# Kernel optimization log

Measured on AMD Instinct MI355X. Metric: run time of the kernel, lower is better.

The kernel has to match this reference:

```python
import jax, jax.numpy as jnp
import numpy as np

B, S, DIN, H, K, DM, DOUT, BANK = 8, 2048, 1024, 2048, 256, 512, 1024, 4096
STICKINESS = 0.1
BANK_SCALE = 4.0
RMS_EPS = 1e-6


def setup_inputs() -> dict:
    key = jax.random.key(0)
    ks = jax.random.split(key, 8)
    s = 0.02
    prev_mode = jnp.zeros((B, K), jnp.float32).at[:, 0].set(1.0)  # default init: mode 0
    return {
        "x": jax.random.normal(ks[0], (B, S, DIN), jnp.float32),
        "prev_mode": prev_mode,
        "Wtr_w": jax.random.normal(ks[1], (DIN, H), jnp.float32) * s,
        "Wtr_b": jnp.zeros((H,), jnp.float32),
        "Wms_w": jax.random.normal(ks[2], (H, K), jnp.float32) * s,
        "Wms_b": jnp.zeros((K,), jnp.float32),
        "M": jax.random.normal(ks[3], (K, DM), jnp.float32) * 0.02,
        "g": jnp.ones((DM,), jnp.float32),
        "Wrd_w": jax.random.normal(ks[4], (DM, DOUT), jnp.float32) * s,
        "Wrd_b": jnp.zeros((DOUT,), jnp.float32),
        "bank_keys": jax.random.normal(ks[5], (BANK, DM), jnp.float32),
        "bank_vals": jax.random.normal(ks[6], (BANK, DM), jnp.float32),
        "bank_used": jnp.ones((BANK,), jnp.float32),
    }


def _l2norm(v):
    n = jnp.sqrt(jnp.sum(v * v, -1, keepdims=True))
    return v / jnp.maximum(n, 1e-12)


def reference(x, prev_mode, Wtr_w, Wtr_b, Wms_w, Wms_b, M, g, Wrd_w, Wrd_b,
              bank_keys, bank_vals, bank_used):
    # Pre-recurrence dense parts (no time dependence): [B,S,H], [B,S,K]
    h = jax.nn.relu(x @ Wtr_w + Wtr_b)
    logits = h @ Wms_w + Wms_b

    # Sequential mode selection with stickiness (eval path: hard argmax one-hot)
    def step(prev, lg):  # prev, lg: [B,K]
        m = jax.nn.one_hot(jnp.argmax(lg + STICKINESS * prev, axis=-1), K, dtype=lg.dtype)
        return m, m

    _, modes = jax.lax.scan(step, prev_mode, jnp.swapaxes(logits, 0, 1))
    modes = jnp.swapaxes(modes, 0, 1)  # [B,S,K]

    mem = modes @ M  # [B,S,DM]

    # Bank read: cosine attention over used slots (masked softmax == torch's slot filtering)
    qn = _l2norm(mem)
    kn = _l2norm(bank_keys)
    scores = jnp.einsum("bsd,nd->bsn", qn, kn) * BANK_SCALE
    scores = jnp.where(bank_used > 0.5, scores, -1e30)
    attn = jax.nn.softmax(scores, axis=-1)
    bank = jnp.einsum("bsn,nd->bsd", attn, bank_vals)

    r = mem + bank
    rn = r * (g / jnp.sqrt(jnp.mean(r * r, -1, keepdims=True) + RMS_EPS))
    y = rn @ Wrd_w + Wrd_b  # [B,S,DOUT]
    return y, modes
```

## Files before the change

kernel.cpp:

```cpp
#include <hip/hip_runtime.h>
#include <stdint.h>

#define ROWS   16384
#define KDIM   256
#define DMDIM  512
#define DOUTD  1024
#define BANKN  4096
#define DIND   1024
#define HDIMD  2048
#define FPAD   1024
#define SCHUNK 64
#define NCHK   32
#define KZ1    4
#define KZ2    8

typedef unsigned int u32;
typedef unsigned short u16;
typedef unsigned char u8;
typedef unsigned long long u64;
typedef _Float16 f16;
typedef _Float16 v8h __attribute__((ext_vector_type(8)));
typedef u16      v8u __attribute__((ext_vector_type(8)));
typedef u16      v4u __attribute__((ext_vector_type(4)));
typedef float    v4f __attribute__((ext_vector_type(4)));

__device__ __forceinline__ u32 pack_split(float v) {
    _Float16 h = (_Float16)v;
    float r = (v - (float)h) * 2048.0f;
    _Float16 l = (_Float16)r;
    u16 hs = __builtin_bit_cast(u16, h);
    u16 ls = __builtin_bit_cast(u16, l);
    return (u32)hs | ((u32)ls << 16);
}
__device__ __forceinline__ v4f mfma16(v8h a, v8h b, v4f c) {
    return __builtin_amdgcn_mfma_f32_16x16x32_f16(a, b, c, 0, 0, 0);
}
__device__ __forceinline__ void gl_lds16(const u32* g, u32* l) {
    __builtin_amdgcn_global_load_lds(g, l, 16, 0, 0);
}

template<bool OSPLIT>
__global__ __launch_bounds__(256, 2)
void gemm_mfma(const f16* __restrict__ A, const f16* __restrict__ Bm_,
               const f16* __restrict__ Br_, const float* __restrict__ bias,
               void* __restrict__ Cv, int K, int kLen)
{
    __shared__ f16 As[128 * 64];
    __shared__ f16 Bs[2 * 128 * 64];
    const int N = gridDim.x * 128;
    const int M = gridDim.y * 128;

    long gx = gridDim.x, gy = gridDim.y, gz = gridDim.z;
    long flat = ((long)blockIdx.z * gy + blockIdx.y) * gx + blockIdx.x;
    long nb = gx * gy * gz;
    long lid = (flat & 7) * (nb >> 3) + (flat >> 3);
    int bx = (int)(lid % gx);
    long t2 = lid / gx;
    int by = (int)(t2 % gy);
    int bz = (int)(t2 / gy);

    const int m0 = by * 128, n0 = bx * 128;
    const int kStart = bz * kLen;

    const int tid = threadIdx.x;
    const int lane = tid & 63, wv = tid >> 6;
    const int lx = lane & 15, q = lane >> 4;
    const int wm = (wv >> 1) * 64, wn = (wv & 1) * 64;

    const int rowb = tid >> 3;
    const int k8   = (tid & 7) ^ (rowb & 7);
    const f16* gA  = A   + (size_t)(m0 + rowb) * K + kStart + k8 * 8;
    const f16* gBm = Bm_ + (size_t)(n0 + rowb) * K + kStart + k8 * 8;
    const f16* gBr = Br_ + (size_t)(n0 + rowb) * K + kStart + k8 * 8;
    f16* lA  = As + (wv * 64) * 8;
    f16* lBm = Bs + (wv * 64) * 8;
    f16* lBr = Bs + 8192 + (wv * 64) * 8;

    int aOff[4][2], bOff[4][2];
    #pragma unroll
    for (int i = 0; i < 4; i++) {
        int ra = wm + i * 16 + lx;
        int rb = wn + i * 16 + lx;
        #pragma unroll
        for (int s = 0; s < 2; s++) {
            aOff[i][s] = ra * 128 + ((s * 64 + q * 16) ^ ((ra & 7) << 4));
            bOff[i][s] = rb * 128 + ((s * 64 + q * 16) ^ ((rb & 7) << 4));
        }
    }

    v4f acc1[4][4], acc2[4][4];
    #pragma unroll
    for (int i = 0; i < 4; i++)
        #pragma unroll
        for (int j = 0; j < 4; j++) { v4f z = {0.f, 0.f, 0.f, 0.f}; acc1[i][j] = z; acc2[i][j] = z; }

    for (int kt = 0; kt < kLen; kt += 64) {
        #pragma unroll
        for (int r = 0; r < 4; r++) {
            gl_lds16((const u32*)(gA  + (size_t)r * 32 * K), (u32*)(lA  + r * 2048));
            gl_lds16((const u32*)(gBm + (size_t)r * 32 * K), (u32*)(lBm + r * 2048));
            gl_lds16((const u32*)(gBr + (size_t)r * 32 * K), (u32*)(lBr + r * 2048));
        }
        gA += 64; gBm += 64; gBr += 64;
        __syncthreads();

        #pragma unroll
        for (int s = 0; s < 2; s++) {
            v8h am[4], bm[4], br[4];
            #pragma unroll
            for (int i = 0; i < 4; i++) {
                am[i] = *(const v8h*)((const char*)As + aOff[i][s]);
                bm[i] = *(const v8h*)((const char*)Bs + bOff[i][s]);
                br[i] = *(const v8h*)((const char*)Bs + 16384 + bOff[i][s]);
            }
            #pragma unroll
            for (int mi = 0; mi < 4; mi++)
                #pragma unroll
                for (int ni = 0; ni < 4; ni++) {
                    acc1[mi][ni] = mfma16(am[mi], bm[ni], acc1[mi][ni]);
                    acc2[mi][ni] = mfma16(am[mi], br[ni], acc2[mi][ni]);
                }
        }
        __syncthreads();
    }

    const float RS = 1.0f / 2048.0f;
    #pragma unroll
    for (int mi = 0; mi < 4; mi++) {
        #pragma unroll
        for (int ni = 0; ni < 4; ni++) {
            int col = n0 + wn + ni * 16 + lx;
            #pragma unroll
            for (int r = 0; r < 4; r++) {
                int row = m0 + wm + mi * 16 + q * 4 + r;
                float v = acc1[mi][ni][r] + acc2[mi][ni][r] * RS;
                if (OSPLIT) {
                    v += bias[col];
                    v = fmaxf(v, 0.f);
                    ((u16*)Cv)[(size_t)row * N + col] = __builtin_bit_cast(u16, (_Float16)v);
                } else {
                    ((float*)Cv)[(size_t)bz * M * N + (size_t)row * N + col] = v;
                }
            }
        }
    }
}

__global__ __launch_bounds__(256)
void packx_k(const float* __restrict__ x, u16* __restrict__ xo, long n8)
{
    long i = (long)blockIdx.x * 256 + threadIdx.x;
    if (i >= n8) return;
    const float4* xp = (const float4*)x;
    float4 a = xp[2 * i], b = xp[2 * i + 1];
    v8u o;
    o[0] = __builtin_bit_cast(u16, (_Float16)a.x);
    o[1] = __builtin_bit_cast(u16, (_Float16)a.y);
    o[2] = __builtin_bit_cast(u16, (_Float16)a.z);
    o[3] = __builtin_bit_cast(u16, (_Float16)a.w);
    o[4] = __builtin_bit_cast(u16, (_Float16)b.x);
    o[5] = __builtin_bit_cast(u16, (_Float16)b.y);
    o[6] = __builtin_bit_cast(u16, (_Float16)b.z);
    o[7] = __builtin_bit_cast(u16, (_Float16)b.w);
    *(v8u*)(xo + i * 8) = o;
}

__global__ __launch_bounds__(256)
void tsplit_k(const float* __restrict__ W, u16* __restrict__ Wm, u16* __restrict__ Wr,
              int K, int N)
{
    __shared__ u32 L[32][33];
    int k0 = blockIdx.y * 32, n0 = blockIdx.x * 32;
    int r = threadIdx.x >> 3, c4 = (threadIdx.x & 7) * 4;
    float4 v = *(const float4*)(W + (size_t)(k0 + r) * N + n0 + c4);
    L[r][c4 + 0] = pack_split(v.x);
    L[r][c4 + 1] = pack_split(v.y);
    L[r][c4 + 2] = pack_split(v.z);
    L[r][c4 + 3] = pack_split(v.w);
    __syncthreads();
    u32 o0 = L[c4 + 0][r], o1 = L[c4 + 1][r], o2 = L[c4 + 2][r], o3 = L[c4 + 3][r];
    v4u mo, ro;
    mo[0] = (u16)o0; mo[1] = (u16)o1; mo[2] = (u16)o2; mo[3] = (u16)o3;
    ro[0] = (u16)(o0 >> 16); ro[1] = (u16)(o1 >> 16); ro[2] = (u16)(o2 >> 16); ro[3] = (u16)(o3 >> 16);
    *(v4u*)(Wm + (size_t)(n0 + r) * K + k0 + c4) = mo;
    *(v4u*)(Wr + (size_t)(n0 + r) * K + k0 + c4) = ro;
}

__global__ __launch_bounds__(256)
void reduce2_k(const float* __restrict__ part, const float* __restrict__ bias,
               float* __restrict__ outp, int total4, int zStride4)
{
    int i = blockIdx.x * 256 + threadIdx.x;
    if (i >= total4) return;
    const float4* p = (const float4*)part;
    float4 s = p[i];
    #pragma unroll
    for (int z = 1; z < 4; z++) {
        float4 t = p[(size_t)z * zStride4 + i];
        s.x += t.x; s.y += t.y; s.z += t.z; s.w += t.w;
    }
    float4 b = ((const float4*)bias)[i & 63];
    s.x += b.x; s.y += b.y; s.z += b.z; s.w += b.w;
    ((float4*)outp)[i] = s;
}

template<bool BT, bool BIAS, bool RELU>
__global__ __launch_bounds__(256)
void gemm64(const float* __restrict__ A, const float* __restrict__ Bm,
            const float* __restrict__ bias, float* __restrict__ C,
            int M, int N, int K, int kLen, const int* __restrict__ mcount)
{
    if (mcount && (int)blockIdx.y * 64 >= *mcount) return;
    __shared__ float As[16][68];
    __shared__ float Bs[16][68];
    const int tid = threadIdx.x;
    const int tx = tid & 15, ty = tid >> 4;
    const int m0 = blockIdx.y * 64;
    const int n0 = blockIdx.x * 64;
    const int z  = blockIdx.z;
    const int kStart = z * kLen;
    float* Cz = C + (size_t)z * M * N;
    float acc[4][4];
    #pragma unroll
    for (int i = 0; i < 4; i++)
        #pragma unroll
        for (int j = 0; j < 4; j++) acc[i][j] = 0.f;

    for (int kt = kStart; kt < kStart + kLen; kt += 16) {
        {
            int m = tid >> 2, kq = tid & 3;
            float4 av = *(const float4*)(A + (size_t)(m0 + m) * K + kt + kq * 4);
            As[kq*4+0][m]=av.x; As[kq*4+1][m]=av.y; As[kq*4+2][m]=av.z; As[kq*4+3][m]=av.w;
        }
        if (BT) {
            int n = tid >> 2, kq = tid & 3;
            float4 bv = *(const float4*)(Bm + (size_t)(n0 + n) * K + kt + kq * 4);
            Bs[kq*4+0][n]=bv.x; Bs[kq*4+1][n]=bv.y; Bs[kq*4+2][n]=bv.z; Bs[kq*4+3][n]=bv.w;
        } else {
            int n4 = tid & 15, kk = tid >> 4;
            float4 bv = *(const float4*)(Bm + (size_t)(kt + kk) * N + n0 + n4 * 4);
            *(float4*)&Bs[kk][n4 * 4] = bv;
        }
        __syncthreads();
        #pragma unroll
        for (int k = 0; k < 16; k++) {
            float4 a0 = *(const float4*)&As[k][ty * 4];
            float4 b0 = *(const float4*)&Bs[k][tx * 4];
            float a[4] = {a0.x, a0.y, a0.z, a0.w};
            float b[4] = {b0.x, b0.y, b0.z, b0.w};
            #pragma unroll
            for (int i = 0; i < 4; i++)
                #pragma unroll
                for (int j = 0; j < 4; j++)
                    acc[i][j] = fmaf(a[i], b[j], acc[i][j]);
        }
        __syncthreads();
    }
    float4 bi = make_float4(0.f,0.f,0.f,0.f);
    if (BIAS) bi = *(const float4*)(bias + n0 + tx * 4);
    #pragma unroll
    for (int i = 0; i < 4; i++) {
        int m = m0 + ty * 4 + i;
        float o0 = acc[i][0]+bi.x, o1 = acc[i][1]+bi.y, o2 = acc[i][2]+bi.z, o3 = acc[i][3]+bi.w;
        if (RELU) { o0=fmaxf(o0,0.f); o1=fmaxf(o1,0.f); o2=fmaxf(o2,0.f); o3=fmaxf(o3,0.f); }
        *(float4*)(Cz + (size_t)m * N + n0 + tx * 4) = make_float4(o0, o1, o2, o3);
    }
}

__global__ __launch_bounds__(64)
void invkn_k(const float* __restrict__ keys, float* __restrict__ inv_kn)
{
    int n = blockIdx.x, l = threadIdx.x;
    const float4* r = (const float4*)(keys + (size_t)n * 512);
    float4 a = r[l], b = r[l + 64];
    float s = a.x*a.x + a.y*a.y + a.z*a.z + a.w*a.w
            + b.x*b.x + b.y*b.y + b.z*b.z + b.w*b.w;
    #pragma unroll
    for (int off = 32; off; off >>= 1) s += __shfl_xor(s, off);
    if (l == 0) inv_kn[n] = 1.0f / fmaxf(sqrtf(s), 1e-12f);
}

__global__ __launch_bounds__(256)
void softmax_k(const float* __restrict__ Mw, const float* __restrict__ inv_kn,
               const float* __restrict__ used, float* __restrict__ sc)
{
    const int k = blockIdx.x, tid = threadIdx.x;
    __shared__ float red[256];
    float m0 = Mw[(size_t)k*512 + tid];
    float m1 = Mw[(size_t)k*512 + 256 + tid];
    red[tid] = m0*m0 + m1*m1;
    __syncthreads();
    for (int s = 128; s > 0; s >>= 1) { if (tid < s) red[tid] += red[tid+s]; __syncthreads(); }
    float scale = 4.0f / fmaxf(sqrtf(red[0]), 1e-12f);
    __syncthreads();
    float vals[16];
    float mx = -3.0e38f;
    #pragma unroll
    for (int j = 0; j < 16; j++) {
        int n = j*256 + tid;
        float v = sc[(size_t)k*4096 + n] * scale * inv_kn[n];
        v = (used[n] > 0.5f) ? v : -1e30f;
        vals[j] = v; mx = fmaxf(mx, v);
    }
    red[tid] = mx; __syncthreads();
    for (int s = 128; s > 0; s >>= 1) { if (tid < s) red[tid] = fmaxf(red[tid], red[tid+s]); __syncthreads(); }
    mx = red[0]; __syncthreads();
    float sum = 0.f;
    #pragma unroll
    for (int j = 0; j < 16; j++) { float e = expf(vals[j] - mx); vals[j] = e; sum += e; }
    red[tid] = sum; __syncthreads();
    for (int s = 128; s > 0; s >>= 1) { if (tid < s) red[tid] += red[tid+s]; __syncthreads(); }
    float inv = 1.0f / red[0];
    #pragma unroll
    for (int j = 0; j < 16; j++) { int n = j*256 + tid; sc[(size_t)k*4096 + n] = vals[j] * inv; }
}

__global__ __launch_bounds__(256)
void redk_k(const float* __restrict__ part, float* __restrict__ outp)
{
    int idx = blockIdx.x * 256 + threadIdx.x;
    float s = 0.f;
    #pragma unroll
    for (int z = 0; z < 8; z++) s += part[(size_t)z * 131072 + idx];
    outp[idx] = s;
}

__global__ __launch_bounds__(256)
void rn_k(const float* __restrict__ Mw, const float* __restrict__ banko,
          const float* __restrict__ g, float* __restrict__ rn)
{
    int k = blockIdx.x, tid = threadIdx.x;
    __shared__ float red[256];
    float r0 = Mw[(size_t)k*512 + tid]       + banko[(size_t)k*512 + tid];
    float r1 = Mw[(size_t)k*512 + 256 + tid] + banko[(size_t)k*512 + 256 + tid];
    red[tid] = r0*r0 + r1*r1;
    __syncthreads();
    for (int s = 128; s > 0; s >>= 1) { if (tid < s) red[tid] += red[tid+s]; __syncthreads(); }
    float denom = sqrtf(red[0] * (1.0f/512.0f) + 1e-6f);
    rn[(size_t)k*512 + tid]       = r0 * (g[tid] / denom);
    rn[(size_t)k*512 + 256 + tid] = r1 * (g[256 + tid] / denom);
}

__global__ __launch_bounds__(64)
void topmask_k(const float* __restrict__ logits, u64* __restrict__ masks,
               int* __restrict__ cArr)
{
    int row = blockIdx.x, l = threadIdx.x;
    const float* lg = logits + (size_t)row * 256;
    float v0 = lg[l], v1 = lg[64 + l], v2 = lg[128 + l], v3 = lg[192 + l];
    float bv = v0; int bp = l;
    if (v1 > bv) { bv = v1; bp = 64 + l; }
    if (v2 > bv) { bv = v2; bp = 128 + l; }
    if (v3 > bv) { bv = v3; bp = 192 + l; }
    #pragma unroll
    for (int off = 32; off; off >>= 1) {
        float ov = __shfl_xor(bv, off);
        int   op = __shfl_xor(bp, off);
        if (ov > bv || (ov == bv && op < bp)) { bv = ov; bp = op; }
    }
    float t0 = v0 + 0.1f, t1 = v1 + 0.1f, t2 = v2 + 0.1f, t3 = v3 + 0.1f;
    u64 w0 = __ballot((t0 > bv) || (t0 == bv && (l)       < bp));
    u64 w1 = __ballot((t1 > bv) || (t1 == bv && (64 + l)  < bp));
    u64 w2 = __ballot((t2 > bv) || (t2 == bv && (128 + l) < bp));
    u64 w3 = __ballot((t3 > bv) || (t3 == bv && (192 + l) < bp));
    if (l == 0) {
        masks[(size_t)row*4 + 0] = w0;
        masks[(size_t)row*4 + 1] = w1;
        masks[(size_t)row*4 + 2] = w2;
        masks[(size_t)row*4 + 3] = w3;
        cArr[row] = bp;
    }
}

__global__ __launch_bounds__(64)
void flag_k(const float* __restrict__ logits, int* __restrict__ flags)
{
    int row = blockIdx.x, l = threadIdx.x;
    const float* lg = logits + (size_t)row * 256;
    float v0 = lg[l], v1 = lg[64 + l], v2 = lg[128 + l], v3 = lg[192 + l];
    float bv = v0; int bp = l;
    if (v1 > bv) { bv = v1; bp = 64 + l; }
    if (v2 > bv) { bv = v2; bp = 128 + l; }
    if (v3 > bv) { bv = v3; bp = 192 + l; }
    #pragma unroll
    for (int off = 32; off; off >>= 1) {
        float ov = __shfl_xor(bv, off);
        int   op = __shfl_xor(bp, off);
        if (ov > bv || (ov == bv && op < bp)) { bv = ov; bp = op; }
    }
    const float D = 1e-3f;
    bool r = false;
    r |= (v0 > bv - D) && ((l)       != bp);  r |= fabsf(v0 + 0.1f - bv) < D;
    r |= (v1 > bv - D) && ((64 + l)  != bp);  r |= fabsf(v1 + 0.1f - bv) < D;
    r |= (v2 > bv - D) && ((128 + l) != bp);  r |= fabsf(v2 + 0.1f - bv) < D;
    r |= (v3 > bv - D) && ((192 + l) != bp);  r |= fabsf(v3 + 0.1f - bv) < D;
    u64 any = __ballot(r);
    if (l == 0) flags[row] = (any != 0ULL) ? 1 : 0;
}

__global__ __launch_bounds__(256)
void compact_k(const int* __restrict__ flags, int* __restrict__ ridx, int* __restrict__ cnt)
{
    int row = blockIdx.x * 256 + threadIdx.x;
    if (row >= ROWS) return;
    if (flags[row]) {
        int p = atomicAdd(cnt, 1);
        if (p < FPAD) ridx[p] = row;
    }
}

__global__ __launch_bounds__(256)
void gatherx_k(const float* __restrict__ x, const int* __restrict__ ridx,
               const int* __restrict__ cnt, float* __restrict__ xg)
{
    int b = blockIdx.x;
    int n = *cnt; if (n > FPAD) n = FPAD;
    if (b >= n) return;
    int row = ridx[b];
    ((float4*)(xg + (size_t)b * 1024))[threadIdx.x] =
        ((const float4*)(x + (size_t)row * 1024))[threadIdx.x];
}

__global__ __launch_bounds__(256)
void redh_k(const float* __restrict__ part, const float* __restrict__ bias,
            const int* __restrict__ cnt, float* __restrict__ hg)
{
    int r = blockIdx.x;
    int n = *cnt; if (n > FPAD) n = FPAD;
    if (r >= n) return;
    int t = threadIdx.x;
    #pragma unroll
    for (int c0 = 0; c0 < HDIMD; c0 += 256) {
        int c = c0 + t;
        float s = part[(size_t)r * HDIMD + c];
        #pragma unroll
        for (int z = 1; z < KZ1; z++)
            s += part[(size_t)z * FPAD * HDIMD + (size_t)r * HDIMD + c];
        hg[(size_t)r * HDIMD + c] = fmaxf(s + bias[c], 0.f);
    }
}

__global__ __launch_bounds__(256)
void redL_k(const float* __restrict__ part, const float* __restrict__ bias,
            const int* __restrict__ ridx, const int* __restrict__ cnt,
            float* __restrict__ logits)
{
    int b = blockIdx.x;
    int n = *cnt; if (n > FPAD) n = FPAD;
    if (b >= n) return;
    int t = threadIdx.x;
    float s = part[(size_t)b * KDIM + t];
    #pragma unroll
    for (int z = 1; z < KZ2; z++)
        s += part[(size_t)z * FPAD * KDIM + (size_t)b * KDIM + t];
    logits[(size_t)ridx[b] * KDIM + t] = s + bias[t];
}

__global__ __launch_bounds__(64)
void scanA_k(const u64* __restrict__ masks, const int* __restrict__ cArr,
             u32* __restrict__ chmap)
{
    int blk = blockIdx.x;
    int l = threadIdx.x;
    int base = blk * 64;
    __shared__ u64 sm[64][4];
    __shared__ int sc[64];
    ulonglong2 m01 = *(const ulonglong2*)(masks + (size_t)(base + l) * 4);
    ulonglong2 m23 = *(const ulonglong2*)(masks + (size_t)(base + l) * 4 + 2);
    sm[l][0] = m01.x; sm[l][1] = m01.y; sm[l][2] = m23.x; sm[l][3] = m23.y;
    sc[l] = cArr[base + l];
    __syncthreads();

    int st[4];
    #pragma unroll
    for (int i = 0; i < 4; i++) st[i] = l * 4 + i;

    for (int j = 0; j < 64; ++j) {
        u64 w0 = sm[j][0], w1 = sm[j][1], w2 = sm[j][2], w3 = sm[j][3];
        int c = sc[j];
        #pragma unroll
        for (int i = 0; i < 4; i++) {
            int s = st[i];
            u64 wlo = (s & 64) ? w1 : w0;
            u64 whi = (s & 64) ? w3 : w2;
            u64 w   = (s & 128) ? whi : wlo;
            int stick = (int)((w >> (s & 63)) & 1ULL);
            st[i] = stick ? s : c;
        }
    }
    u32 outv = (u32)(st[0] & 255) | ((u32)(st[1] & 255) << 8)
             | ((u32)(st[2] & 255) << 16) | ((u32)(st[3] & 255) << 24);
    chmap[(size_t)blk * 64 + l] = outv;
}

__global__ __launch_bounds__(64)
void scanB_k(const u32* __restrict__ chmap, const float* __restrict__ prev_mode,
             int* __restrict__ entry)
{
    int b = blockIdx.x, l = threadIdx.x;
    __shared__ u8 lm[NCHK * 256];
    const u32* src = chmap + (size_t)b * NCHK * 64;
    #pragma unroll
    for (int i = 0; i < NCHK; ++i) ((u32*)lm)[i * 64 + l] = src[i * 64 + l];

    float4 pm = ((const float4*)(prev_mode + (size_t)b * 256))[l];
    int my = -1;
    if (pm.x > 0.5f) my = l * 4 + 0;
    if (pm.y > 0.5f) my = l * 4 + 1;
    if (pm.z > 0.5f) my = l * 4 + 2;
    if (pm.w > 0.5f) my = l * 4 + 3;
    u64 bal = __ballot(my >= 0);
    int prev = 0;
    if (bal) {
        int s2 = __ffsll(bal) - 1;
        prev = __builtin_amdgcn_readlane(my, s2);
    }
    __syncthreads();
    if (l == 0) {
        int e = prev;
        for (int ci = 0; ci < NCHK; ++ci) {
            entry[b * NCHK + ci] = e;
            e = lm[ci * 256 + e];
        }
    }
}

__global__ __launch_bounds__(64)
void scanC_k(const u64* __restrict__ masks, const int* __restrict__ cArr,
             const int* __restrict__ entry, int* __restrict__ midx)
{
    int blk = blockIdx.x, l = threadIdx.x;
    int base = blk * 64;
    ulonglong2 c01 = *(const ulonglong2*)(masks + (size_t)(base + l) * 4);
    ulonglong2 c23 = *(const ulonglong2*)(masks + (size_t)(base + l) * 4 + 2);
    int cc = cArr[base + l];
    int prev = entry[blk];
    int myres = 0;
    for (int j = 0; j < 64; ++j) {
        u64 wlo = (prev & 64) ? c01.y : c01.x;
        u64 whi = (prev & 64) ? c23.y : c23.x;
        u64 w   = (prev & 128) ? whi : wlo;
        unsigned int lo32 = (unsigned int)__builtin_amdgcn_readlane((int)(unsigned int)w, j);
        unsigned int hi32 = (unsigned int)__builtin_amdgcn_readlane((int)(unsigned int)(w >> 32), j);
        int c = __builtin_amdgcn_readlane(cc, j);
        u64 ww = ((u64)hi32 << 32) | (u64)lo32;
        int stick = (int)((ww >> (prev & 63)) & 1ULL);
        prev = stick ? prev : c;
        myres = (l == j) ? prev : myres;
    }
    midx[base + l] = myres;
}

__global__ __launch_bounds__(64)
void modesw_k(const int* __restrict__ mode_idx, float* __restrict__ modes)
{
    int r = blockIdx.x, l = threadIdx.x;
    int k = mode_idx[r];
    int base = l * 4;
    float4 v = make_float4(base == k ? 1.f : 0.f, base+1 == k ? 1.f : 0.f,
                           base+2 == k ? 1.f : 0.f, base+3 == k ? 1.f : 0.f);
    ((float4*)(modes + (size_t)r * 256))[l] = v;
}

__global__ __launch_bounds__(256)
void ygather_k(const int* __restrict__ mode_idx, const float* __restrict__ ytab,
               float* __restrict__ y)
{
    int r = blockIdx.x;
    int k = mode_idx[r];
    const float4* src = (const float4*)(ytab + (size_t)k * 1024);
    float4* dst = (float4*)(y + (size_t)r * 1024);
    dst[threadIdx.x] = src[threadIdx.x];
}

extern "C" void kernel_launch(void* const* d_in, const int* in_sizes, int n_in,
                              void* d_out, int out_size, void* d_ws, size_t ws_size,
                              hipStream_t stream)
{
    const float* x       = (const float*)d_in[0];
    const float* prevm   = (const float*)d_in[1];
    const float* Wtr_w   = (const float*)d_in[2];
    const float* Wtr_b   = (const float*)d_in[3];
    const float* Wms_w   = (const float*)d_in[4];
    const float* Wms_b   = (const float*)d_in[5];
    const float* Mw      = (const float*)d_in[6];
    const float* g       = (const float*)d_in[7];
    const float* Wrd_w   = (const float*)d_in[8];
    const float* Wrd_b   = (const float*)d_in[9];
    const float* bkeys   = (const float*)d_in[10];
    const float* bvals   = (const float*)d_in[11];
    const float* bused   = (const float*)d_in[12];

    float* y_out     = (float*)d_out;
    float* modes_out = y_out + (size_t)ROWS * DOUTD;

    char* w = (char*)d_ws;
    size_t o = 0;
    auto alloc = [&](size_t b) { size_t r = o; o = (o + b + 255) & ~(size_t)255; return r; };

    size_t oLog  = alloc((size_t)ROWS * 256 * 4);
    size_t oMask = alloc((size_t)ROWS * 32);
    size_t oCar  = alloc((size_t)ROWS * 4);
    size_t oMidx = alloc((size_t)ROWS * 4);
    size_t oInv  = alloc((size_t)BANKN * 4);
    size_t oSc   = alloc((size_t)256 * 4096 * 4);
    size_t oPB   = alloc((size_t)8 * 256 * 512 * 4);
    size_t oBo   = alloc((size_t)256 * 512 * 4);
    size_t oRn   = alloc((size_t)256 * 512 * 4);
    size_t oYt   = alloc((size_t)256 * 1024 * 4);
    size_t oW1m  = alloc((size_t)HDIMD * DIND * 2);
    size_t oW1r  = alloc((size_t)HDIMD * DIND * 2);
    size_t oW2m  = alloc((size_t)KDIM * HDIMD * 2);
    size_t oW2r  = alloc((size_t)KDIM * HDIMD * 2);
    size_t oChm  = alloc((size_t)8 * NCHK * 256);
    size_t oEnt  = alloc((size_t)8 * NCHK * 4);
    size_t oFlag = alloc((size_t)ROWS * 4);
    size_t oRidx = alloc((size_t)FPAD * 4);
    size_t oCnt  = alloc(256);
    size_t oXg   = alloc((size_t)FPAD * DIND * 4);
    size_t oHP   = alloc((size_t)KZ1 * FPAD * HDIMD * 4);
    size_t oHg   = alloc((size_t)FPAD * HDIMD * 4);
    size_t oLP   = alloc((size_t)KZ2 * FPAD * KDIM * 4);
    size_t persist = o;

    int CM = 256;
    const int cands[7] = {16384, 8192, 4096, 2048, 1024, 512, 256};
    for (int i = 0; i < 7; i++) {
        size_t need = persist + (size_t)cands[i] * 10240 + 1024;
        if (need <= ws_size) { CM = cands[i]; break; }
    }
    size_t oXi = alloc((size_t)CM * DIND * 2);
    size_t oHi = alloc((size_t)CM * HDIMD * 2);
    size_t oP2 = alloc((size_t)4 * CM * 256 * 4);

    float* logits = (float*)(w + oLog);
    u64*   masks  = (u64*)(w + oMask);
    int*   cArr   = (int*)(w + oCar);
    int*   midx   = (int*)(w + oMidx);
    float* invkn  = (float*)(w + oInv);
    float* scores = (float*)(w + oSc);
    float* partB  = (float*)(w + oPB);
    float* banko  = (float*)(w + oBo);
    float* rn     = (float*)(w + oRn);
    float* ytab   = (float*)(w + oYt);
    u16*   W1m    = (u16*)(w + oW1m);
    u16*   W1r    = (u16*)(w + oW1r);
    u16*   W2m    = (u16*)(w + oW2m);
    u16*   W2r    = (u16*)(w + oW2r);
    u32*   chmap  = (u32*)(w + oChm);
    int*   entry  = (int*)(w + oEnt);
    int*   flags  = (int*)(w + oFlag);
    int*   ridx   = (int*)(w + oRidx);
    int*   cnt    = (int*)(w + oCnt);
    float* xg     = (float*)(w + oXg);
    float* hPart  = (float*)(w + oHP);
    float* hg     = (float*)(w + oHg);
    float* lPart  = (float*)(w + oLP);
    u16*   xi     = (u16*)(w + oXi);
    u16*   hi     = (u16*)(w + oHi);
    float* part2  = (float*)(w + oP2);

    invkn_k<<<BANKN, 64, 0, stream>>>(bkeys, invkn);
    gemm64<true, false, false><<<dim3(64, 4, 1), 256, 0, stream>>>(Mw, bkeys, nullptr, scores,
                                                                   256, 4096, 512, 512, nullptr);
    softmax_k<<<KDIM, 256, 0, stream>>>(Mw, invkn, bused, scores);
    gemm64<false, false, false><<<dim3(8, 4, 8), 256, 0, stream>>>(scores, bvals, nullptr, partB,
                                                                   256, 512, 4096, 512, nullptr);
    redk_k<<<512, 256, 0, stream>>>(partB, banko);
    rn_k<<<KDIM, 256, 0, stream>>>(Mw, banko, g, rn);
    gemm64<false, true, false><<<dim3(16, 4, 1), 256, 0, stream>>>(rn, Wrd_w, Wrd_b, ytab,
                                                                   256, 1024, 512, 512, nullptr);

    tsplit_k<<<dim3(HDIMD / 32, DIND / 32), 256, 0, stream>>>(Wtr_w, W1m, W1r, DIND, HDIMD);
    tsplit_k<<<dim3(KDIM / 32, HDIMD / 32), 256, 0, stream>>>(Wms_w, W2m, W2r, HDIMD, KDIM);

    for (int ch0 = 0; ch0 < ROWS; ch0 += CM) {
        long n8 = (long)CM * DIND / 8;
        packx_k<<<(int)((n8 + 255) / 256), 256, 0, stream>>>(x + (size_t)ch0 * DIND, xi, n8);
        gemm_mfma<true><<<dim3(HDIMD / 128, CM / 128, 1), 256, 0, stream>>>(
            (const f16*)xi, (const f16*)W1m, (const f16*)W1r, Wtr_b, hi, DIND, DIND);
        gemm_mfma<false><<<dim3(KDIM / 128, CM / 128, 4), 256, 0, stream>>>(
            (const f16*)hi, (const f16*)W2m, (const f16*)W2r, nullptr, part2, HDIMD, HDIMD / 4);
        int total4 = CM * 256 / 4;
        reduce2_k<<<(total4 + 255) / 256, 256, 0, stream>>>(part2, Wms_b,
            logits + (size_t)ch0 * 256, total4, total4);
    }

    flag_k<<<ROWS, 64, 0, stream>>>(logits, flags);
    hipMemsetAsync(cnt, 0, 4, stream);
    compact_k<<<ROWS / 256, 256, 0, stream>>>(flags, ridx, cnt);
    gatherx_k<<<FPAD, 256, 0, stream>>>(x, ridx, cnt, xg);
    gemm64<false, false, false><<<dim3(HDIMD / 64, FPAD / 64, KZ1), 256, 0, stream>>>(
        xg, Wtr_w, nullptr, hPart, FPAD, HDIMD, DIND, DIND / KZ1, cnt);
    redh_k<<<FPAD, 256, 0, stream>>>(hPart, Wtr_b, cnt, hg);
    gemm64<false, false, false><<<dim3(KDIM / 64, FPAD / 64, KZ2), 256, 0, stream>>>(
        hg, Wms_w, nullptr, lPart, FPAD, KDIM, HDIMD, HDIMD / KZ2, cnt);
    redL_k<<<FPAD, 256, 0, stream>>>(lPart, Wms_b, ridx, cnt, logits);

    topmask_k<<<ROWS, 64, 0, stream>>>(logits, masks, cArr);
    scanA_k<<<8 * NCHK, 64, 0, stream>>>(masks, cArr, chmap);
    scanB_k<<<8, 64, 0, stream>>>(chmap, prevm, entry);
    scanC_k<<<8 * NCHK, 64, 0, stream>>>(masks, cArr, entry, midx);

    modesw_k<<<ROWS, 64, 0, stream>>>(midx, modes_out);
    ygather_k<<<ROWS, 256, 0, stream>>>(midx, ytab, y_out);
}
```

Measured before the change: 592.6 us.

## Move bank-read GEMMs to split-fp16 MFMA and halve split-K for logits

```diff
diff --git a/kernel.cpp b/kernel.cpp
--- a/kernel.cpp
+++ b/kernel.cpp
@@ -11,7 +11,7 @@
 #define FPAD   1024
 #define SCHUNK 64
 #define NCHK   32
-#define KZ1    4
+#define KZ1    2
 #define KZ2    8
 
 typedef unsigned int u32;
@@ -20,6 +20,7 @@
 typedef unsigned long long u64;
 typedef _Float16 f16;
 typedef _Float16 v8h __attribute__((ext_vector_type(8)));
+typedef short    v8s __attribute__((ext_vector_type(8)));
 typedef u16      v8u __attribute__((ext_vector_type(8)));
 typedef u16      v4u __attribute__((ext_vector_type(4)));
 typedef float    v4f __attribute__((ext_vector_type(4)));
@@ -31,6 +32,18 @@
     u16 hs = __builtin_bit_cast(u16, h);
     u16 ls = __builtin_bit_cast(u16, l);
     return (u32)hs | ((u32)ls << 16);
+}
+__device__ __forceinline__ v8h unpL(uint4 a, uint4 b) {
+    v8s s1 = __builtin_bit_cast(v8s, a);
+    v8s s2 = __builtin_bit_cast(v8s, b);
+    v8s lo = __builtin_shufflevector(s1, s2, 0, 2, 4, 6, 8, 10, 12, 14);
+    return __builtin_bit_cast(v8h, lo);
+}
+__device__ __forceinline__ v8h unpH(uint4 a, uint4 b) {
+    v8s s1 = __builtin_bit_cast(v8s, a);
+    v8s s2 = __builtin_bit_cast(v8s, b);
+    v8s hi = __builtin_shufflevector(s1, s2, 1, 3, 5, 7, 9, 11, 13, 15);
+    return __builtin_bit_cast(v8h, hi);
 }
 __device__ __forceinline__ v4f mfma16(v8h a, v8h b, v4f c) {
     return __builtin_amdgcn_mfma_f32_16x16x32_f16(a, b, c, 0, 0, 0);
@@ -146,6 +159,104 @@
     }
 }
 
+template<bool BIASF>
+__global__ __launch_bounds__(256, 2)
+void gemm_sp3(const u32* __restrict__ A, const u32* __restrict__ Bt,
+              const float* __restrict__ bias, float* __restrict__ Cv,
+              int K, int kLen)
+{
+    __shared__ u32 As[4096];
+    __shared__ u32 Bs[4096];
+    const int N = gridDim.x * 128;
+    const int M = gridDim.y * 128;
+
+    long gx = gridDim.x, gy = gridDim.y, gz = gridDim.z;
+    long flat = ((long)blockIdx.z * gy + blockIdx.y) * gx + blockIdx.x;
+    long nb = gx * gy * gz;
+    long lid = (flat & 7) * (nb >> 3) + (flat >> 3);
+    int bx = (int)(lid % gx);
+    long t2 = lid / gx;
+    int by = (int)(t2 % gy);
+    int bz = (int)(t2 / gy);
+
+    const int m0 = by * 128, n0 = bx * 128;
+    const int kStart = bz * kLen;
+
+    const int tid = threadIdx.x;
+    const int lane = tid & 63, wv = tid >> 6;
+    const int lx = lane & 15, q = lane >> 4;
+    const int wm = (wv >> 1) * 64, wn = (wv & 1) * 64;
+
+    const u32* gA = A + (size_t)(m0 + (tid >> 6) * 8 + (tid & 7)) * K + kStart + ((tid >> 3) & 7) * 4;
+    const u32* gB = Bt + (size_t)(n0 + (tid >> 6) * 8 + (tid & 7)) * K + kStart + ((tid >> 3) & 7) * 4;
+    u32* lA = As + (wv * 64) * 4;
+    u32* lB = Bs + (wv * 64) * 4;
+
+    int caOff[4], cbOff[4];
+    #pragma unroll
+    for (int i = 0; i < 4; i++) {
+        int m = wm + i * 16 + lx;
+        caOff[i] = (((m >> 3) * 64) + q * 16 + (m & 7)) * 4;
+        int n = wn + i * 16 + lx;
+        cbOff[i] = (((n >> 3) * 64) + q * 16 + (n & 7)) * 4;
+    }
+
+    v4f acc1[4][4], acc2[4][4];
+    #pragma unroll
+    for (int i = 0; i < 4; i++)
+        #pragma unroll
+        for (int j = 0; j < 4; j++) { v4f z = {0.f, 0.f, 0.f, 0.f}; acc1[i][j] = z; acc2[i][j] = z; }
+
+    for (int kt = 0; kt < kLen; kt += 32) {
+        #pragma unroll
+        for (int r = 0; r < 4; r++) {
+            gl_lds16(gA + (size_t)r * 32 * K, lA + r * 1024);
+            gl_lds16(gB + (size_t)r * 32 * K, lB + r * 1024);
+        }
+        gA += 32; gB += 32;
+        __syncthreads();
+
+        v8h am[4], ar[4], bm[4], br[4];
+        #pragma unroll
+        for (int i = 0; i < 4; i++) {
+            uint4 x1 = *(const uint4*)(As + caOff[i]);
+            uint4 x2 = *(const uint4*)(As + caOff[i] + 32);
+            am[i] = unpL(x1, x2); ar[i] = unpH(x1, x2);
+            uint4 y1 = *(const uint4*)(Bs + cbOff[i]);
+            uint4 y2 = *(const uint4*)(Bs + cbOff[i] + 32);
+            bm[i] = unpL(y1, y2); br[i] = unpH(y1, y2);
+        }
+        #pragma unroll
+        for (int mi = 0; mi < 4; mi++)
+            #pragma unroll
+            for (int ni = 0; ni < 4; ni++) {
+                acc1[mi][ni] = mfma16(am[mi], bm[ni], acc1[mi][ni]);
+                acc2[mi][ni] = mfma16(am[mi], br[ni], acc2[mi][ni]);
+                acc2[mi][ni] = mfma16(ar[mi], bm[ni], acc2[mi][ni]);
+            }
+        __syncthreads();
+    }
+
+    const float RS = 1.0f / 2048.0f;
+    #pragma unroll
+    for (int mi = 0; mi < 4; mi++) {
+        #pragma unroll
+        for (int ni = 0; ni < 4; ni++) {
+            int col = n0 + wn + ni * 16 + lx;
+            #pragma unroll
+            for (int r = 0; r < 4; r++) {
+                int row = m0 + wm + mi * 16 + q * 4 + r;
+                float v = acc1[mi][ni][r] + acc2[mi][ni][r] * RS;
+                if (BIASF) {
+                    Cv[(size_t)row * N + col] = v + bias[col];
+                } else {
+                    Cv[(size_t)bz * M * N + (size_t)row * N + col] = v;
+                }
+            }
+        }
+    }
+}
+
 __global__ __launch_bounds__(256)
 void packx_k(const float* __restrict__ x, u16* __restrict__ xo, long n8)
 {
@@ -163,6 +274,35 @@
     o[6] = __builtin_bit_cast(u16, (_Float16)b.z);
     o[7] = __builtin_bit_cast(u16, (_Float16)b.w);
     *(v8u*)(xo + i * 8) = o;
+}
+
+__global__ __launch_bounds__(256)
+void packrow_k(const float* __restrict__ x, u32* __restrict__ xi, long n4)
+{
+    long i = (long)blockIdx.x * 256 + threadIdx.x;
+    if (i >= n4) return;
+    float4 v = ((const float4*)x)[i];
+    uint4 o;
+    o.x = pack_split(v.x); o.y = pack_split(v.y);
+    o.z = pack_split(v.z); o.w = pack_split(v.w);
+    ((uint4*)xi)[i] = o;
+}
+
+__global__ __launch_bounds__(256)
+void tpack_k(const float* __restrict__ W, u32* __restrict__ Wt, int K, int N)
+{
+    __shared__ u32 L[32][33];
+    int k0 = blockIdx.y * 32, n0 = blockIdx.x * 32;
+    int r = threadIdx.x >> 3, c4 = (threadIdx.x & 7) * 4;
+    float4 v = *(const float4*)(W + (size_t)(k0 + r) * N + n0 + c4);
+    L[r][c4 + 0] = pack_split(v.x);
+    L[r][c4 + 1] = pack_split(v.y);
+    L[r][c4 + 2] = pack_split(v.z);
+    L[r][c4 + 3] = pack_split(v.w);
+    __syncthreads();
+    uint4 ov;
+    ov.x = L[c4 + 0][r]; ov.y = L[c4 + 1][r]; ov.z = L[c4 + 2][r]; ov.w = L[c4 + 3][r];
+    *(uint4*)(Wt + (size_t)(n0 + r) * K + k0 + c4) = ov;
 }
 
 __global__ __launch_bounds__(256)
@@ -188,14 +328,13 @@
 
 __global__ __launch_bounds__(256)
 void reduce2_k(const float* __restrict__ part, const float* __restrict__ bias,
-               float* __restrict__ outp, int total4, int zStride4)
+               float* __restrict__ outp, int total4, int zStride4, int zc)
 {
     int i = blockIdx.x * 256 + threadIdx.x;
     if (i >= total4) return;
     const float4* p = (const float4*)part;
     float4 s = p[i];
-    #pragma unroll
-    for (int z = 1; z < 4; z++) {
+    for (int z = 1; z < zc; z++) {
         float4 t = p[(size_t)z * zStride4 + i];
         s.x += t.x; s.y += t.y; s.z += t.z; s.w += t.w;
     }
@@ -612,6 +751,12 @@
     size_t oW1r  = alloc((size_t)HDIMD * DIND * 2);
     size_t oW2m  = alloc((size_t)KDIM * HDIMD * 2);
     size_t oW2r  = alloc((size_t)KDIM * HDIMD * 2);
+    size_t oMwP  = alloc((size_t)KDIM * DMDIM * 4);
+    size_t oBkP  = alloc((size_t)BANKN * DMDIM * 4);
+    size_t oAtP  = alloc((size_t)KDIM * BANKN * 4);
+    size_t oBvP  = alloc((size_t)DMDIM * BANKN * 4);
+    size_t oRnP  = alloc((size_t)KDIM * DMDIM * 4);
+    size_t oWrdP = alloc((size_t)DOUTD * DMDIM * 4);
     size_t oChm  = alloc((size_t)8 * NCHK * 256);
     size_t oEnt  = alloc((size_t)8 * NCHK * 4);
     size_t oFlag = alloc((size_t)ROWS * 4);
@@ -626,12 +771,12 @@
     int CM = 256;
     const int cands[7] = {16384, 8192, 4096, 2048, 1024, 512, 256};
     for (int i = 0; i < 7; i++) {
-        size_t need = persist + (size_t)cands[i] * 10240 + 1024;
+        size_t need = persist + (size_t)cands[i] * 8192 + 1024;
         if (need <= ws_size) { CM = cands[i]; break; }
     }
     size_t oXi = alloc((size_t)CM * DIND * 2);
     size_t oHi = alloc((size_t)CM * HDIMD * 2);
-    size_t oP2 = alloc((size_t)4 * CM * 256 * 4);
+    size_t oP2 = alloc((size_t)2 * CM * 256 * 4);
 
     float* logits = (float*)(w + oLog);
     u64*   masks  = (u64*)(w + oMask);
@@ -647,6 +792,12 @@
     u16*   W1r    = (u16*)(w + oW1r);
     u16*   W2m    = (u16*)(w + oW2m);
     u16*   W2r    = (u16*)(w + oW2r);
+    u32*   MwP    = (u32*)(w + oMwP);
+    u32*   bkP    = (u32*)(w + oBkP);
+    u32*   atP    = (u32*)(w + oAtP);
+    u32*   bvP    = (u32*)(w + oBvP);
+    u32*   rnP    = (u32*)(w + oRnP);
+    u32*   WrdP   = (u32*)(w + oWrdP);
     u32*   chmap  = (u32*)(w + oChm);
     int*   entry  = (int*)(w + oEnt);
     int*   flags  = (int*)(w + oFlag);
@@ -661,15 +812,21 @@
     float* part2  = (float*)(w + oP2);
 
     invkn_k<<<BANKN, 64, 0, stream>>>(bkeys, invkn);
-    gemm64<true, false, false><<<dim3(64, 4, 1), 256, 0, stream>>>(Mw, bkeys, nullptr, scores,
-                                                                   256, 4096, 512, 512, nullptr);
+    packrow_k<<<(KDIM * DMDIM / 4 + 255) / 256, 256, 0, stream>>>(Mw, MwP, KDIM * DMDIM / 4);
+    packrow_k<<<(BANKN * DMDIM / 4 + 255) / 256, 256, 0, stream>>>(bkeys, bkP, BANKN * DMDIM / 4);
+    tpack_k<<<dim3(DMDIM / 32, BANKN / 32), 256, 0, stream>>>(bvals, bvP, BANKN, DMDIM);
+    tpack_k<<<dim3(DOUTD / 32, DMDIM / 32), 256, 0, stream>>>(Wrd_w, WrdP, DMDIM, DOUTD);
+    gemm_sp3<false><<<dim3(BANKN / 128, KDIM / 128, 1), 256, 0, stream>>>(
+        MwP, bkP, nullptr, scores, DMDIM, DMDIM);
     softmax_k<<<KDIM, 256, 0, stream>>>(Mw, invkn, bused, scores);
-    gemm64<false, false, false><<<dim3(8, 4, 8), 256, 0, stream>>>(scores, bvals, nullptr, partB,
-                                                                   256, 512, 4096, 512, nullptr);
+    packrow_k<<<(KDIM * BANKN / 4 + 255) / 256, 256, 0, stream>>>(scores, atP, KDIM * BANKN / 4);
+    gemm_sp3<false><<<dim3(DMDIM / 128, KDIM / 128, 8), 256, 0, stream>>>(
+        atP, bvP, nullptr, partB, BANKN, BANKN / 8);
     redk_k<<<512, 256, 0, stream>>>(partB, banko);
     rn_k<<<KDIM, 256, 0, stream>>>(Mw, banko, g, rn);
-    gemm64<false, true, false><<<dim3(16, 4, 1), 256, 0, stream>>>(rn, Wrd_w, Wrd_b, ytab,
-                                                                   256, 1024, 512, 512, nullptr);
+    packrow_k<<<(KDIM * DMDIM / 4 + 255) / 256, 256, 0, stream>>>(rn, rnP, KDIM * DMDIM / 4);
+    gemm_sp3<true><<<dim3(DOUTD / 128, KDIM / 128, 1), 256, 0, stream>>>(
+        rnP, WrdP, Wrd_b, ytab, DMDIM, DMDIM);
 
     tsplit_k<<<dim3(HDIMD / 32, DIND / 32), 256, 0, stream>>>(Wtr_w, W1m, W1r, DIND, HDIMD);
     tsplit_k<<<dim3(KDIM / 32, HDIMD / 32), 256, 0, stream>>>(Wms_w, W2m, W2r, HDIMD, KDIM);
@@ -679,11 +836,11 @@
         packx_k<<<(int)((n8 + 255) / 256), 256, 0, stream>>>(x + (size_t)ch0 * DIND, xi, n8);
         gemm_mfma<true><<<dim3(HDIMD / 128, CM / 128, 1), 256, 0, stream>>>(
             (const f16*)xi, (const f16*)W1m, (const f16*)W1r, Wtr_b, hi, DIND, DIND);
-        gemm_mfma<false><<<dim3(KDIM / 128, CM / 128, 4), 256, 0, stream>>>(
-            (const f16*)hi, (const f16*)W2m, (const f16*)W2r, nullptr, part2, HDIMD, HDIMD / 4);
+        gemm_mfma<false><<<dim3(KDIM / 128, CM / 128, 2), 256, 0, stream>>>(
+            (const f16*)hi, (const f16*)W2m, (const f16*)W2r, nullptr, part2, HDIMD, HDIMD / 2);
         int total4 = CM * 256 / 4;
         reduce2_k<<<(total4 + 255) / 256, 256, 0, stream>>>(part2, Wms_b,
-            logits + (size_t)ch0 * 256, total4, total4);
+            logits + (size_t)ch0 * 256, total4, total4, 2);
     }
 
     flag_k<<<ROWS, 64, 0, stream>>>(logits, flags);
```

New measurement: 624.2 us. 1.05x slower.

## Fuse fp32-to-fp16 conversion into GEMM A-load and merge small row kernels

Applied to the files above, without the earlier changes.

```diff
diff --git a/kernel.cpp b/kernel.cpp
--- a/kernel.cpp
+++ b/kernel.cpp
@@ -39,9 +39,9 @@
     __builtin_amdgcn_global_load_lds(g, l, 16, 0, 0);
 }
 
-template<bool OSPLIT>
+template<bool OSPLIT, bool AF32>
 __global__ __launch_bounds__(256, 2)
-void gemm_mfma(const f16* __restrict__ A, const f16* __restrict__ Bm_,
+void gemm_mfma(const void* __restrict__ Av, const f16* __restrict__ Bm_,
                const f16* __restrict__ Br_, const float* __restrict__ bias,
                void* __restrict__ Cv, int K, int kLen)
 {
@@ -69,12 +69,14 @@
 
     const int rowb = tid >> 3;
     const int k8   = (tid & 7) ^ (rowb & 7);
-    const f16* gA  = A   + (size_t)(m0 + rowb) * K + kStart + k8 * 8;
+    const f16*  gA  = AF32 ? nullptr : (const f16*)Av + (size_t)(m0 + rowb) * K + kStart + k8 * 8;
+    const float* gAf = AF32 ? (const float*)Av + (size_t)(m0 + rowb) * K + kStart + (tid & 7) * 8 : nullptr;
     const f16* gBm = Bm_ + (size_t)(n0 + rowb) * K + kStart + k8 * 8;
     const f16* gBr = Br_ + (size_t)(n0 + rowb) * K + kStart + k8 * 8;
     f16* lA  = As + (wv * 64) * 8;
     f16* lBm = Bs + (wv * 64) * 8;
     f16* lBr = Bs + 8192 + (wv * 64) * 8;
+    const int aw = rowb * 64 + k8 * 8;
 
     int aOff[4][2], bOff[4][2];
     #pragma unroll
@@ -95,13 +97,42 @@
         for (int j = 0; j < 4; j++) { v4f z = {0.f, 0.f, 0.f, 0.f}; acc1[i][j] = z; acc2[i][j] = z; }
 
     for (int kt = 0; kt < kLen; kt += 64) {
-        #pragma unroll
-        for (int r = 0; r < 4; r++) {
-            gl_lds16((const u32*)(gA  + (size_t)r * 32 * K), (u32*)(lA  + r * 2048));
-            gl_lds16((const u32*)(gBm + (size_t)r * 32 * K), (u32*)(lBm + r * 2048));
-            gl_lds16((const u32*)(gBr + (size_t)r * 32 * K), (u32*)(lBr + r * 2048));
-        }
-        gA += 64; gBm += 64; gBr += 64;
+        if (AF32) {
+            float4 fa[4][2];
+            #pragma unroll
+            for (int r = 0; r < 4; r++) {
+                fa[r][0] = *(const float4*)(gAf + (size_t)r * 32 * K);
+                fa[r][1] = *(const float4*)(gAf + (size_t)r * 32 * K + 4);
+            }
+            gAf += 64;
+            #pragma unroll
+            for (int r = 0; r < 4; r++) {
+                gl_lds16((const u32*)(gBm + (size_t)r * 32 * K), (u32*)(lBm + r * 2048));
+                gl_lds16((const u32*)(gBr + (size_t)r * 32 * K), (u32*)(lBr + r * 2048));
+            }
+            #pragma unroll
+            for (int r = 0; r < 4; r++) {
+                v8u o;
+                o[0] = __builtin_bit_cast(u16, (_Float16)fa[r][0].x);
+                o[1] = __builtin_bit_cast(u16, (_Float16)fa[r][0].y);
+                o[2] = __builtin_bit_cast(u16, (_Float16)fa[r][0].z);
+                o[3] = __builtin_bit_cast(u16, (_Float16)fa[r][0].w);
+                o[4] = __builtin_bit_cast(u16, (_Float16)fa[r][1].x);
+                o[5] = __builtin_bit_cast(u16, (_Float16)fa[r][1].y);
+                o[6] = __builtin_bit_cast(u16, (_Float16)fa[r][1].z);
+                o[7] = __builtin_bit_cast(u16, (_Float16)fa[r][1].w);
+                *(v8u*)(As + aw + r * 2048) = o;
+            }
+        } else {
+            #pragma unroll
+            for (int r = 0; r < 4; r++) {
+                gl_lds16((const u32*)(gA  + (size_t)r * 32 * K), (u32*)(lA  + r * 2048));
+                gl_lds16((const u32*)(gBm + (size_t)r * 32 * K), (u32*)(lBm + r * 2048));
+                gl_lds16((const u32*)(gBr + (size_t)r * 32 * K), (u32*)(lBr + r * 2048));
+            }
+            gA += 64;
+        }
+        gBm += 64; gBr += 64;
         __syncthreads();
 
         #pragma unroll
@@ -144,25 +175,6 @@
             }
         }
     }
-}
-
-__global__ __launch_bounds__(256)
-void packx_k(const float* __restrict__ x, u16* __restrict__ xo, long n8)
-{
-    long i = (long)blockIdx.x * 256 + threadIdx.x;
-    if (i >= n8) return;
-    const float4* xp = (const float4*)x;
-    float4 a = xp[2 * i], b = xp[2 * i + 1];
-    v8u o;
-    o[0] = __builtin_bit_cast(u16, (_Float16)a.x);
-    o[1] = __builtin_bit_cast(u16, (_Float16)a.y);
-    o[2] = __builtin_bit_cast(u16, (_Float16)a.z);
-    o[3] = __builtin_bit_cast(u16, (_Float16)a.w);
-    o[4] = __builtin_bit_cast(u16, (_Float16)b.x);
-    o[5] = __builtin_bit_cast(u16, (_Float16)b.y);
-    o[6] = __builtin_bit_cast(u16, (_Float16)b.z);
-    o[7] = __builtin_bit_cast(u16, (_Float16)b.w);
-    *(v8u*)(xo + i * 8) = o;
 }
 
 __global__ __launch_bounds__(256)
@@ -188,14 +200,13 @@
 
 __global__ __launch_bounds__(256)
 void reduce2_k(const float* __restrict__ part, const float* __restrict__ bias,
-               float* __restrict__ outp, int total4, int zStride4)
+               float* __restrict__ outp, int total4, int zStride4, int zc)
 {
     int i = blockIdx.x * 256 + threadIdx.x;
     if (i >= total4) return;
     const float4* p = (const float4*)part;
     float4 s = p[i];
-    #pragma unroll
-    for (int z = 1; z < 4; z++) {
+    for (int z = 1; z < zc; z++) {
         float4 t = p[(size_t)z * zStride4 + i];
         s.x += t.x; s.y += t.y; s.z += t.z; s.w += t.w;
     }
@@ -342,8 +353,8 @@
 }
 
 __global__ __launch_bounds__(64)
-void topmask_k(const float* __restrict__ logits, u64* __restrict__ masks,
-               int* __restrict__ cArr)
+void topflag_k(const float* __restrict__ logits, u64* __restrict__ masks,
+               int* __restrict__ cArr, int* __restrict__ flags)
 {
     int row = blockIdx.x, l = threadIdx.x;
     const float* lg = logits + (size_t)row * 256;
@@ -363,39 +374,21 @@
     u64 w1 = __ballot((t1 > bv) || (t1 == bv && (64 + l)  < bp));
     u64 w2 = __ballot((t2 > bv) || (t2 == bv && (128 + l) < bp));
     u64 w3 = __ballot((t3 > bv) || (t3 == bv && (192 + l) < bp));
+    const float D = 1e-3f;
+    bool r = false;
+    r |= (v0 > bv - D) && ((l)       != bp);  r |= fabsf(t0 - bv) < D;
+    r |= (v1 > bv - D) && ((64 + l)  != bp);  r |= fabsf(t1 - bv) < D;
+    r |= (v2 > bv - D) && ((128 + l) != bp);  r |= fabsf(t2 - bv) < D;
+    r |= (v3 > bv - D) && ((192 + l) != bp);  r |= fabsf(t3 - bv) < D;
+    u64 any = __ballot(r);
     if (l == 0) {
         masks[(size_t)row*4 + 0] = w0;
         masks[(size_t)row*4 + 1] = w1;
         masks[(size_t)row*4 + 2] = w2;
         masks[(size_t)row*4 + 3] = w3;
         cArr[row] = bp;
-    }
-}
-
-__global__ __launch_bounds__(64)
-void flag_k(const float* __restrict__ logits, int* __restrict__ flags)
-{
-    int row = blockIdx.x, l = threadIdx.x;
-    const float* lg = logits + (size_t)row * 256;
-    float v0 = lg[l], v1 = lg[64 + l], v2 = lg[128 + l], v3 = lg[192 + l];
-    float bv = v0; int bp = l;
-    if (v1 > bv) { bv = v1; bp = 64 + l; }
-    if (v2 > bv) { bv = v2; bp = 128 + l; }
-    if (v3 > bv) { bv = v3; bp = 192 + l; }
-    #pragma unroll
-    for (int off = 32; off; off >>= 1) {
-        float ov = __shfl_xor(bv, off);
-        int   op = __shfl_xor(bp, off);
-        if (ov > bv || (ov == bv && op < bp)) { bv = ov; bp = op; }
-    }
-    const float D = 1e-3f;
-    bool r = false;
-    r |= (v0 > bv - D) && ((l)       != bp);  r |= fabsf(v0 + 0.1f - bv) < D;
-    r |= (v1 > bv - D) && ((64 + l)  != bp);  r |= fabsf(v1 + 0.1f - bv) < D;
-    r |= (v2 > bv - D) && ((128 + l) != bp);  r |= fabsf(v2 + 0.1f - bv) < D;
-    r |= (v3 > bv - D) && ((192 + l) != bp);  r |= fabsf(v3 + 0.1f - bv) < D;
-    u64 any = __ballot(r);
-    if (l == 0) flags[row] = (any != 0ULL) ? 1 : 0;
+        flags[row] = (any != 0ULL) ? 1 : 0;
+    }
 }
 
 __global__ __launch_bounds__(256)
@@ -551,26 +544,20 @@
     midx[base + l] = myres;
 }
 
-__global__ __launch_bounds__(64)
-void modesw_k(const int* __restrict__ mode_idx, float* __restrict__ modes)
-{
-    int r = blockIdx.x, l = threadIdx.x;
+__global__ __launch_bounds__(256)
+void yout_k(const int* __restrict__ mode_idx, const float* __restrict__ ytab,
+            float* __restrict__ y, float* __restrict__ modes)
+{
+    int r = blockIdx.x, t = threadIdx.x;
     int k = mode_idx[r];
-    int base = l * 4;
-    float4 v = make_float4(base == k ? 1.f : 0.f, base+1 == k ? 1.f : 0.f,
-                           base+2 == k ? 1.f : 0.f, base+3 == k ? 1.f : 0.f);
-    ((float4*)(modes + (size_t)r * 256))[l] = v;
-}
-
-__global__ __launch_bounds__(256)
-void ygather_k(const int* __restrict__ mode_idx, const float* __restrict__ ytab,
-               float* __restrict__ y)
-{
-    int r = blockIdx.x;
-    int k = mode_idx[r];
-    const float4* src = (const float4*)(ytab + (size_t)k * 1024);
-    float4* dst = (float4*)(y + (size_t)r * 1024);
-    dst[threadIdx.x] = src[threadIdx.x];
+    ((float4*)(y + (size_t)r * 1024))[t] =
+        ((const float4*)(ytab + (size_t)k * 1024))[t];
+    if (t < 64) {
+        int base = t * 4;
+        float4 v = make_float4(base == k ? 1.f : 0.f, base+1 == k ? 1.f : 0.f,
+                               base+2 == k ? 1.f : 0.f, base+3 == k ? 1.f : 0.f);
+        ((float4*)(modes + (size_t)r * 256))[t] = v;
+    }
 }
 
 extern "C" void kernel_launch(void* const* d_in, const int* in_sizes, int n_in,
@@ -626,10 +613,9 @@
     int CM = 256;
     const int cands[7] = {16384, 8192, 4096, 2048, 1024, 512, 256};
     for (int i = 0; i < 7; i++) {
-        size_t need = persist + (size_t)cands[i] * 10240 + 1024;
+        size_t need = persist + (size_t)cands[i] * 8192 + 1024;
         if (need <= ws_size) { CM = cands[i]; break; }
     }
-    size_t oXi = alloc((size_t)CM * DIND * 2);
     size_t oHi = alloc((size_t)CM * HDIMD * 2);
     size_t oP2 = alloc((size_t)4 * CM * 256 * 4);
 
@@ -656,7 +642,6 @@
     float* hPart  = (float*)(w + oHP);
     float* hg     = (float*)(w + oHg);
     float* lPart  = (float*)(w + oLP);
-    u16*   xi     = (u16*)(w + oXi);
     u16*   hi     = (u16*)(w + oHi);
     float* part2  = (float*)(w + oP2);
 
@@ -675,18 +660,17 @@
     tsplit_k<<<dim3(KDIM / 32, HDIMD / 32), 256, 0, stream>>>(Wms_w, W2m, W2r, HDIMD, KDIM);
 
     for (int ch0 = 0; ch0 < ROWS; ch0 += CM) {
-        long n8 = (long)CM * DIND / 8;
-        packx_k<<<(int)((n8 + 255) / 256), 256, 0, stream>>>(x + (size_t)ch0 * DIND, xi, n8);
-        gemm_mfma<true><<<dim3(HDIMD / 128, CM / 128, 1), 256, 0, stream>>>(
-            (const f16*)xi, (const f16*)W1m, (const f16*)W1r, Wtr_b, hi, DIND, DIND);
-        gemm_mfma<false><<<dim3(KDIM / 128, CM / 128, 4), 256, 0, stream>>>(
-            (const f16*)hi, (const f16*)W2m, (const f16*)W2r, nullptr, part2, HDIMD, HDIMD / 4);
+        gemm_mfma<true, true><<<dim3(HDIMD / 128, CM / 128, 1), 256, 0, stream>>>(
+            (const void*)(x + (size_t)ch0 * DIND), (const f16*)W1m, (const f16*)W1r,
+            Wtr_b, hi, DIND, DIND);
+        gemm_mfma<false, false><<<dim3(KDIM / 128, CM / 128, 4), 256, 0, stream>>>(
+            (const void*)hi, (const f16*)W2m, (const f16*)W2r, nullptr, part2, HDIMD, HDIMD / 4);
         int total4 = CM * 256 / 4;
         reduce2_k<<<(total4 + 255) / 256, 256, 0, stream>>>(part2, Wms_b,
-            logits + (size_t)ch0 * 256, total4, total4);
-    }
-
-    flag_k<<<ROWS, 64, 0, stream>>>(logits, flags);
+            logits + (size_t)ch0 * 256, total4, total4, 4);
+    }
+
+    topflag_k<<<ROWS, 64, 0, stream>>>(logits, masks, cArr, flags);
     hipMemsetAsync(cnt, 0, 4, stream);
     compact_k<<<ROWS / 256, 256, 0, stream>>>(flags, ridx, cnt);
     gatherx_k<<<FPAD, 256, 0, stream>>>(x, ridx, cnt, xg);
@@ -696,12 +680,11 @@
     gemm64<false, false, false><<<dim3(KDIM / 64, FPAD / 64, KZ2), 256, 0, stream>>>(
         hg, Wms_w, nullptr, lPart, FPAD, KDIM, HDIMD, HDIMD / KZ2, cnt);
     redL_k<<<FPAD, 256, 0, stream>>>(lPart, Wms_b, ridx, cnt, logits);
-
-    topmask_k<<<ROWS, 64, 0, stream>>>(logits, masks, cArr);
+    topflag_k<<<ROWS, 64, 0, stream>>>(logits, masks, cArr, flags);
+
     scanA_k<<<8 * NCHK, 64, 0, stream>>>(masks, cArr, chmap);
     scanB_k<<<8, 64, 0, stream>>>(chmap, prevm, entry);
     scanC_k<<<8 * NCHK, 64, 0, stream>>>(masks, cArr, entry, midx);
 
-    modesw_k<<<ROWS, 64, 0, stream>>>(midx, modes_out);
-    ygather_k<<<ROWS, 256, 0, stream>>>(midx, ytab, y_out);
-}
+    yout_k<<<ROWS, 256, 0, stream>>>(midx, ytab, y_out, modes_out);
+}
```

After: 620.7 us. 4.7% more time.
